# Kernel optimization log

Measured on AMD Instinct MI355X. Metric: run time of the kernel, lower is better.

## Reference

```python
import jax, jax.numpy as jnp
import numpy as np

B, S, D, H, HD, I = 8, 512, 2048, 32, 64, 8192
REL = 2 * 512 - 1  # 1023
EPS = 1e-6
SCALE = float(np.sqrt(HD))


def _layernorm(x, g, b):
    mu = jnp.mean(x, axis=-1, keepdims=True)
    var = jnp.mean(jnp.square(x - mu), axis=-1, keepdims=True)
    return (x - mu) / jnp.sqrt(var + EPS) * g + b


def setup_inputs() -> dict:
    key = jax.random.key(0)
    ks = jax.random.split(key, 10)
    s = 0.02
    return {
        "hidden_states": jax.random.normal(ks[0], (B, S, D), dtype=jnp.float32),
        "wq": jax.random.normal(ks[1], (D, D), dtype=jnp.float32) * s,
        "wk": jax.random.normal(ks[2], (D, D), dtype=jnp.float32) * s,
        "wv": jax.random.normal(ks[3], (D, D), dtype=jnp.float32) * s,
        "wo": jax.random.normal(ks[4], (D, D), dtype=jnp.float32) * s,
        "rel_pos": jax.random.normal(ks[5], (REL, HD), dtype=jnp.float32),
        "ln1_g": jnp.ones((D,), jnp.float32),
        "ln1_b": jnp.zeros((D,), jnp.float32),
        "gate_w": jax.random.normal(ks[6], (D, I), dtype=jnp.float32) * s,
        "up_w": jax.random.normal(ks[7], (D, I), dtype=jnp.float32) * s,
        "down_w": jax.random.normal(ks[8], (I, D), dtype=jnp.float32) * s,
        "ln2_g": jnp.ones((D,), jnp.float32),
        "ln2_b": jnp.zeros((D,), jnp.float32),
    }


def reference(hidden_states, wq, wk, wv, wo, rel_pos, ln1_g, ln1_b,
              gate_w, up_w, down_w, ln2_g, ln2_b):
    x = hidden_states
    # --- MultiHeadAttentionXL ---
    q = (x @ wq).reshape(B, S, H, HD)
    k = (x @ wk).reshape(B, S, H, HD)
    v = (x @ wv).reshape(B, S, H, HD)
    scores = jnp.einsum('bqhd,bkhd->bhqk', q, k) / SCALE
    # relative position bias (seq_len <= 512 path)
    pos = jnp.arange(S)
    rp = jnp.clip(pos[None, :] - pos[:, None] + 512 - 1, 0, REL - 1)  # [S,S]
    bias = rel_pos[rp].mean(axis=-1)  # [S,S]
    scores = scores + bias[None, None]
    attn = jax.nn.softmax(scores, axis=-1)
    ctx = jnp.einsum('bhqk,bkhd->bqhd', attn, v).reshape(B, S, D)
    attn_out = ctx @ wo
    # residual + post-LN
    h = _layernorm(x + attn_out, ln1_g, ln1_b)
    # --- FeedForwardXL (SwiGLU) ---
    gate = jax.nn.silu(h @ gate_w)
    up = h @ up_w
    ffn = (gate * up) @ down_w
    h = _layernorm(h + ffn, ln2_g, ln2_b)
    return h
```

## Files before the change

### kernel.cpp

```cpp
#include <hip/hip_runtime.h>
#include <cstdint>
#include <cstddef>

typedef _Float16 f16;
typedef _Float16 f16x8 __attribute__((ext_vector_type(8)));
typedef _Float16 f16x4 __attribute__((ext_vector_type(4)));
typedef float    f32x4 __attribute__((ext_vector_type(4)));

constexpr int S_ = 512, D_ = 2048, H_ = 32, HD_ = 64, I_ = 8192;
constexpr int M_ = 4096;
constexpr int IH_ = 4096;

enum { OP_F32 = 0, OP_QKT = 3, OP_PV = 4, OP_QKV = 6, OP_GU = 9, OP_ADD = 10 };

__device__ __forceinline__ void gl_lds16(const void* g, void* lds) {
  __builtin_amdgcn_global_load_lds(
      (const __attribute__((address_space(1))) void*)g,
      (__attribute__((address_space(3))) void*)lds, 16, 0, 0);
}

template <int BM, int BN, int WR, int WC, int OP>
__global__ __launch_bounds__(256, 2) void gemm_k(
    const f16* __restrict__ A, int lda,
    const f16* __restrict__ B, int ldb,
    void* __restrict__ Cp, int ldc,
    int K, int bh0, const float* __restrict__ relmean,
    const f16* __restrict__ B2) {
  constexpr int BK = 32;
  constexpr bool GU = (OP == OP_GU);
  constexpr int WM = BM / WR, WN = BN / WC;
  constexpr int IM = WM / 16, IN = WN / 16;
  constexpr int CA = BM / 64, CB = BN / 64;
  __shared__ __align__(16) f16 As[BM * BK];
  __shared__ __align__(16) f16 Bs[(GU ? 2 : 1) * BN * BK];
  const int tid = threadIdx.x, wave = tid >> 6, lane = tid & 63;
  const int wm = wave / WC, wn = wave % WC;
  const int bn = blockIdx.x, bm = blockIdx.y, bz = blockIdx.z;

  long aoff = 0, boff = 0;
  if constexpr (OP == OP_QKT) {
    int bh = bh0 + bz;
    long hb = (long)(bh >> 5) * (S_ * D_) + (long)(bh & (H_ - 1)) * HD_;
    aoff = hb; boff = hb;
  }
  if constexpr (OP == OP_PV) {
    int bh = bh0 + bz;
    aoff = (long)bz * S_ * S_;
    boff = (long)bh * HD_ * S_;
  }
  if constexpr (OP == OP_QKV) boff = (long)bz * D_ * D_;

  const f16* Ab = A + aoff + (long)bm * BM * lda;
  const f16* Bb = B + boff + (long)bn * BN * ldb;
  const f16* Bb2 = nullptr;
  if constexpr (GU) Bb2 = B2 + (long)bn * BN * ldb;

  f32x4 acc[IM][IN], acc2[IM][IN];
#pragma unroll
  for (int i = 0; i < IM; i++)
#pragma unroll
    for (int j = 0; j < IN; j++) {
      acc[i][j] = {0.f, 0.f, 0.f, 0.f};
      if constexpr (GU) acc2[i][j] = {0.f, 0.f, 0.f, 0.f};
    }

  const int lr = lane >> 2, l4 = lane & 3;
  const int q8 = (lane >> 4) * 8, l15 = lane & 15;

  for (int kt = 0; kt < K; kt += BK) {
#pragma unroll
    for (int c = 0; c < CA; c++) {
      int reg = wave * CA + c;
      gl_lds16(Ab + (long)(reg * 16 + lr) * lda + kt + l4 * 8, &As[reg * 512]);
    }
#pragma unroll
    for (int c = 0; c < CB; c++) {
      int reg = wave * CB + c;
      gl_lds16(Bb + (long)(reg * 16 + lr) * ldb + kt + l4 * 8, &Bs[reg * 512]);
      if constexpr (GU)
        gl_lds16(Bb2 + (long)(reg * 16 + lr) * ldb + kt + l4 * 8,
                 &Bs[BN * BK + reg * 512]);
    }
    __syncthreads();
    f16x8 af[IM], bf[IN], bf2[IN];
#pragma unroll
    for (int i = 0; i < IM; i++)
      af[i] = *(const f16x8*)&As[(wm * WM + i * 16 + l15) * BK + q8];
#pragma unroll
    for (int j = 0; j < IN; j++) {
      int colL = wn * WN + j * 16 + l15;
      bf[j] = *(const f16x8*)&Bs[colL * BK + q8];
      if constexpr (GU) bf2[j] = *(const f16x8*)&Bs[BN * BK + colL * BK + q8];
    }
#pragma unroll
    for (int i = 0; i < IM; i++)
#pragma unroll
      for (int j = 0; j < IN; j++) {
        acc[i][j] = __builtin_amdgcn_mfma_f32_16x16x32_f16(af[i], bf[j], acc[i][j], 0, 0, 0);
        if constexpr (GU)
          acc2[i][j] = __builtin_amdgcn_mfma_f32_16x16x32_f16(af[i], bf2[j], acc2[i][j], 0, 0, 0);
      }
    __syncthreads();
  }

  const int r0 = bm * BM + wm * WM + (lane >> 4) * 4;
  const int c0 = bn * BN + wn * WN + l15;
#pragma unroll
  for (int i = 0; i < IM; i++) {
#pragma unroll
    for (int j = 0; j < IN; j++) {
      int rowb = r0 + i * 16;
      int col = c0 + j * 16;
      if constexpr (OP == OP_F32) {
        float* C = (float*)Cp;
#pragma unroll
        for (int t = 0; t < 4; t++) C[(long)(rowb + t) * ldc + col] = acc[i][j][t];
      } else if constexpr (OP == OP_ADD) {
        float* C = (float*)Cp;
#pragma unroll
        for (int t = 0; t < 4; t++) C[(long)(rowb + t) * ldc + col] += acc[i][j][t];
      } else if constexpr (OP == OP_GU) {
        f16* C = (f16*)Cp;
#pragma unroll
        for (int t = 0; t < 4; t++) {
          float g = acc[i][j][t], u = acc2[i][j][t];
          C[(long)(rowb + t) * ldc + col] = (f16)(g / (1.f + __expf(-g)) * u);
        }
      } else if constexpr (OP == OP_QKT) {
        f16* C = (f16*)Cp + (long)bz * S_ * S_;
#pragma unroll
        for (int t = 0; t < 4; t++) {
          int r = rowb + t;
          C[(long)r * S_ + col] = (f16)(acc[i][j][t] * 0.125f + relmean[col - r + 511]);
        }
      } else if constexpr (OP == OP_PV) {
        int bh = bh0 + bz;
        f16* C = (f16*)Cp + (long)(bh >> 5) * (S_ * D_) + (long)(bh & (H_ - 1)) * HD_;
#pragma unroll
        for (int t = 0; t < 4; t++) C[(long)(rowb + t) * ldc + col] = (f16)acc[i][j][t];
      } else if constexpr (OP == OP_QKV) {
        f16* C = (f16*)Cp;
        if (bz < 2) {
          f16* Cq = C + (long)bz * M_ * D_;
#pragma unroll
          for (int t = 0; t < 4; t++) Cq[(long)(rowb + t) * ldc + col] = (f16)acc[i][j][t];
        } else {
          f16* Cv = C + (long)2 * M_ * D_;
          int b = rowb >> 9, s0 = rowb & 511, h = col >> 6, hd = col & 63;
          f16x4 pk;
#pragma unroll
          for (int t = 0; t < 4; t++) pk[t] = (f16)acc[i][j][t];
          *(f16x4*)&Cv[((long)(b * H_ + h) * HD_ + hd) * S_ + s0] = pk;
        }
      }
    }
  }
}

__global__ __launch_bounds__(256) void transpose_k(
    const float* __restrict__ in, int ldin, int k0, int n0,
    f16* __restrict__ out, int ldout) {
  __shared__ f16 t[64][68];
  const int kb = blockIdx.x * 64, nb = blockIdx.y * 64;
  const int tid = threadIdx.x;
  {
    const int kr = tid >> 4, nc = (tid & 15) * 4;
    const float* src = in + (long)(k0 + kb) * ldin + (n0 + nb);
#pragma unroll
    for (int i = 0; i < 4; i++) {
      int k = kr + i * 16;
      f32x4 v = *(const f32x4*)&src[(long)k * ldin + nc];
#pragma unroll
      for (int j = 0; j < 4; j++) t[nc + j][k] = (f16)v[j];
    }
  }
  __syncthreads();
  {
    const int n = tid >> 2, kc = (tid & 3) * 16;
    f16* dst = out + (long)(nb + n) * ldout + (kb + kc);
#pragma unroll
    for (int j = 0; j < 4; j++)
      *(f16x4*)&dst[j * 4] = *(const f16x4*)&t[n][kc + j * 4];
  }
}

__global__ void cvt_f16_k(const float* __restrict__ in, f16* __restrict__ out, int n4) {
  int i = blockIdx.x * 256 + threadIdx.x;
  if (i >= n4) return;
  f32x4 v = ((const f32x4*)in)[i];
  f16x4 o;
#pragma unroll
  for (int t = 0; t < 4; t++) o[t] = (f16)v[t];
  ((f16x4*)out)[i] = o;
}

__global__ void relmean_k(const float* __restrict__ rel, float* __restrict__ rm) {
  int i = blockIdx.x * 256 + threadIdx.x;
  if (i >= 1023) return;
  float s = 0.f;
#pragma unroll 8
  for (int d = 0; d < 64; d++) s += rel[i * 64 + d];
  rm[i] = s * (1.f / 64.f);
}

__global__ __launch_bounds__(256) void softmax_k(f16* __restrict__ Sc) {
  int r = blockIdx.x * 4 + (threadIdx.x >> 6);
  int lane = threadIdx.x & 63;
  f16* s = Sc + (long)r * S_;
  f16x8 d = *(const f16x8*)&s[lane * 8];
  float v[8], mx = -1e30f;
#pragma unroll
  for (int i = 0; i < 8; i++) { v[i] = (float)d[i]; mx = fmaxf(mx, v[i]); }
  for (int off = 32; off; off >>= 1) mx = fmaxf(mx, __shfl_xor(mx, off));
  float sum = 0.f;
#pragma unroll
  for (int i = 0; i < 8; i++) { v[i] = __expf(v[i] - mx); sum += v[i]; }
  for (int off = 32; off; off >>= 1) sum += __shfl_xor(sum, off);
  float rs = 1.f / sum;
  f16x8 o;
#pragma unroll
  for (int i = 0; i < 8; i++) o[i] = (f16)(v[i] * rs);
  *(f16x8*)&s[lane * 8] = o;
}

__global__ __launch_bounds__(256) void ln1_k(const float* __restrict__ X,
                                             const float* __restrict__ Y,
                                             const float* __restrict__ g,
                                             const float* __restrict__ b,
                                             f16* __restrict__ outH) {
  int row = blockIdx.x;
  const float* x = X + (long)row * D_;
  const float* y = Y + (long)row * D_;
  int t = threadIdx.x;
  float v[8], sum = 0.f, sq = 0.f;
#pragma unroll
  for (int i = 0; i < 8; i++) {
    int idx = t + i * 256;
    float val = x[idx] + y[idx];
    v[i] = val; sum += val; sq += val * val;
  }
  for (int off = 32; off; off >>= 1) { sum += __shfl_down(sum, off); sq += __shfl_down(sq, off); }
  __shared__ float s1[4], s2[4];
  if ((t & 63) == 0) { s1[t >> 6] = sum; s2[t >> 6] = sq; }
  __syncthreads();
  sum = s1[0] + s1[1] + s1[2] + s1[3];
  sq = s2[0] + s2[1] + s2[2] + s2[3];
  float mu = sum * (1.f / D_);
  float rstd = rsqrtf(sq * (1.f / D_) - mu * mu + 1e-6f);
#pragma unroll
  for (int i = 0; i < 8; i++) {
    int idx = t + i * 256;
    outH[(long)row * D_ + idx] = (f16)((v[i] - mu) * rstd * g[idx] + b[idx]);
  }
}

__global__ __launch_bounds__(256) void ln2f_k(const float* __restrict__ X,
                                              const f16* __restrict__ Y,
                                              const float* __restrict__ g,
                                              const float* __restrict__ b,
                                              float* __restrict__ outF) {
  int row = blockIdx.x;
  const float* x = X + (long)row * D_;
  const f16* y = Y + (long)row * D_;
  int t = threadIdx.x;
  float v[8], sum = 0.f, sq = 0.f;
#pragma unroll
  for (int i = 0; i < 8; i++) {
    int idx = t + i * 256;
    float val = x[idx] + (float)y[idx];
    v[i] = val; sum += val; sq += val * val;
  }
  for (int off = 32; off; off >>= 1) { sum += __shfl_down(sum, off); sq += __shfl_down(sq, off); }
  __shared__ float s1[4], s2[4];
  if ((t & 63) == 0) { s1[t >> 6] = sum; s2[t >> 6] = sq; }
  __syncthreads();
  sum = s1[0] + s1[1] + s1[2] + s1[3];
  sq = s2[0] + s2[1] + s2[2] + s2[3];
  float mu = sum * (1.f / D_);
  float rstd = rsqrtf(sq * (1.f / D_) - mu * mu + 1e-6f);
#pragma unroll
  for (int i = 0; i < 8; i++) {
    int idx = t + i * 256;
    outF[(long)row * D_ + idx] = (v[i] - mu) * rstd * g[idx] + b[idx];
  }
}

extern "C" void kernel_launch(void* const* d_in, const int* in_sizes, int n_in,
                              void* d_out, int out_size, void* d_ws, size_t ws_size,
                              hipStream_t stream) {
  const float* x    = (const float*)d_in[0];
  const float* wq   = (const float*)d_in[1];
  const float* wk   = (const float*)d_in[2];
  const float* wv   = (const float*)d_in[3];
  const float* wo   = (const float*)d_in[4];
  const float* rel  = (const float*)d_in[5];
  const float* ln1g = (const float*)d_in[6];
  const float* ln1b = (const float*)d_in[7];
  const float* gw   = (const float*)d_in[8];
  const float* uw   = (const float*)d_in[9];
  const float* dw   = (const float*)d_in[10];
  const float* ln2g = (const float*)d_in[11];
  const float* ln2b = (const float*)d_in[12];
  float* out = (float*)d_out;

  constexpr size_t MD2 = (size_t)M_ * D_ * 2;
  if (ws_size < 8 * MD2 + 4096) return;
  char* w = (char*)d_ws;
  f16* qb   = (f16*)(w + 0 * MD2);
  f16* vT   = (f16*)(w + 2 * MD2);
  f16* xb   = (f16*)(w + 3 * MD2);
  f16* sc   = (f16*)(w + 4 * MD2);
  f16* h1h  = (f16*)(w + 6 * MD2);
  f16* s7   = (f16*)(w + 7 * MD2);
  float* relmean = (float*)(w + 8 * MD2);
  f16* ctxb = xb;
  float* attn_out = (float*)qb;
  f16* wqT  = sc;
  f16* woT  = s7;
  f16* gwTh = qb;
  f16* uwTh = (f16*)(w + 1 * MD2);
  f16* gch  = vT;
  f16* dwTh = s7;
  float* facc = (float*)sc;

  cvt_f16_k<<<M_ * D_ / 4 / 256, 256, 0, stream>>>(x, xb, M_ * D_ / 4);
  relmean_k<<<4, 256, 0, stream>>>(rel, relmean);
  transpose_k<<<dim3(32, 32), 256, 0, stream>>>(wq, D_, 0, 0, wqT, D_);
  transpose_k<<<dim3(32, 32), 256, 0, stream>>>(wk, D_, 0, 0, wqT + (size_t)D_ * D_, D_);
  transpose_k<<<dim3(32, 32), 256, 0, stream>>>(wv, D_, 0, 0, wqT + 2 * (size_t)D_ * D_, D_);
  transpose_k<<<dim3(32, 32), 256, 0, stream>>>(wo, D_, 0, 0, woT, D_);

  gemm_k<128, 128, 2, 2, OP_QKV><<<dim3(16, 32, 3), 256, 0, stream>>>(
      xb, D_, wqT, D_, qb, D_, D_, 0, nullptr, nullptr);

  for (int c = 0; c < 4; c++) {
    int bh0 = c * 64;
    gemm_k<128, 128, 2, 2, OP_QKT><<<dim3(4, 4, 64), 256, 0, stream>>>(
        qb, D_, qb + (size_t)M_ * D_, D_, sc, S_, HD_, bh0, relmean, nullptr);
    softmax_k<<<64 * S_ / 4, 256, 0, stream>>>(sc);
    gemm_k<64, 64, 2, 2, OP_PV><<<dim3(1, 8, 64), 256, 0, stream>>>(
        sc, S_, vT, S_, ctxb, D_, S_, bh0, nullptr, nullptr);
  }

  gemm_k<128, 128, 2, 2, OP_F32><<<dim3(16, 32, 1), 256, 0, stream>>>(
      ctxb, D_, woT, D_, attn_out, D_, D_, 0, nullptr, nullptr);
  ln1_k<<<M_, 256, 0, stream>>>(x, attn_out, ln1g, ln1b, h1h);

  for (int h = 0; h < 2; h++) {
    transpose_k<<<dim3(32, 64), 256, 0, stream>>>(gw, I_, 0, h * IH_, gwTh, D_);
    transpose_k<<<dim3(32, 64), 256, 0, stream>>>(uw, I_, 0, h * IH_, uwTh, D_);
    transpose_k<<<dim3(64, 32), 256, 0, stream>>>(dw, D_, h * IH_, 0, dwTh, IH_);
    gemm_k<128, 64, 2, 2, OP_GU><<<dim3(IH_ / 64, 32, 1), 256, 0, stream>>>(
        h1h, D_, gwTh, D_, gch, IH_, D_, 0, nullptr, uwTh);
    if (h == 0)
      gemm_k<128, 128, 2, 2, OP_F32><<<dim3(16, 32, 1), 256, 0, stream>>>(
          gch, IH_, dwTh, IH_, facc, D_, IH_, 0, nullptr, nullptr);
    else
      gemm_k<128, 128, 2, 2, OP_ADD><<<dim3(16, 32, 1), 256, 0, stream>>>(
          gch, IH_, dwTh, IH_, facc, D_, IH_, 0, nullptr, nullptr);
  }
  ln2f_k<<<M_, 256, 0, stream>>>(facc, h1h, ln2g, ln2b, out);
}
```

Measured before the change: 1.249 ms.

## Add BK=64 swizzled LDS tiles for attention GEMMs and widen gate/up tile

Makes the GEMM K-tile depth a template parameter. A BK=64 variant uses an XOR-swizzled LDS layout to avoid bank conflicts, and the attention QK^T and PV GEMMs now use it. The end-of-loop barrier moves to the start of the next iteration. The gate/up SwiGLU GEMM goes from a 128x64 to a 128x128 tile with half the blocks, which raises reuse of the A tile. The larger tile doubles accumulators in the GU kernel, which risks register pressure and lower occupancy.

```diff
diff --git a/kernel.cpp b/kernel.cpp
--- a/kernel.cpp
+++ b/kernel.cpp
@@ -19,18 +19,22 @@
       (__attribute__((address_space(3))) void*)lds, 16, 0, 0);
 }
 
-template <int BM, int BN, int WR, int WC, int OP>
+template <int BM, int BN, int WR, int WC, int OP, int BK>
 __global__ __launch_bounds__(256, 2) void gemm_k(
     const f16* __restrict__ A, int lda,
     const f16* __restrict__ B, int ldb,
     void* __restrict__ Cp, int ldc,
     int K, int bh0, const float* __restrict__ relmean,
     const f16* __restrict__ B2) {
-  constexpr int BK = 32;
+  static_assert(WR * WC == 4, "4-wave blocks assumed");
+  static_assert(BK == 32 || BK == 64, "");
   constexpr bool GU = (OP == OP_GU);
   constexpr int WM = BM / WR, WN = BN / WC;
   constexpr int IM = WM / 16, IN = WN / 16;
-  constexpr int CA = BM / 64, CB = BN / 64;
+  constexpr int RR = (BK == 64) ? 8 : 16;
+  constexpr int CA = BM * BK / 2048;
+  constexpr int CB = BN * BK / 2048;
+  constexpr int KS = BK / 32;
   __shared__ __align__(16) f16 As[BM * BK];
   __shared__ __align__(16) f16 Bs[(GU ? 2 : 1) * BN * BK];
   const int tid = threadIdx.x, wave = tid >> 6, lane = tid & 63;
@@ -55,7 +59,7 @@
   const f16* Bb2 = nullptr;
   if constexpr (GU) Bb2 = B2 + (long)bn * BN * ldb;
 
-  f32x4 acc[IM][IN], acc2[IM][IN];
+  f32x4 acc[IM][IN], acc2[GU ? IM : 1][GU ? IN : 1];
 #pragma unroll
   for (int i = 0; i < IM; i++)
 #pragma unroll
@@ -64,43 +68,56 @@
       if constexpr (GU) acc2[i][j] = {0.f, 0.f, 0.f, 0.f};
     }
 
-  const int lr = lane >> 2, l4 = lane & 3;
-  const int q8 = (lane >> 4) * 8, l15 = lane & 15;
+  const int lrr = (BK == 64) ? (lane >> 3) : (lane >> 2);
+  const int lcc = (BK == 64) ? (lane & 7) : (lane & 3);
+  const int scc = (BK == 64) ? (lcc ^ (lrr & 7)) : lcc;
+  const int g = lane >> 4, l15 = lane & 15;
 
   for (int kt = 0; kt < K; kt += BK) {
+    if (kt) __syncthreads();
 #pragma unroll
     for (int c = 0; c < CA; c++) {
       int reg = wave * CA + c;
-      gl_lds16(Ab + (long)(reg * 16 + lr) * lda + kt + l4 * 8, &As[reg * 512]);
+      gl_lds16(Ab + (long)(reg * RR + lrr) * lda + kt + scc * 8, &As[reg * 512]);
     }
 #pragma unroll
     for (int c = 0; c < CB; c++) {
       int reg = wave * CB + c;
-      gl_lds16(Bb + (long)(reg * 16 + lr) * ldb + kt + l4 * 8, &Bs[reg * 512]);
+      gl_lds16(Bb + (long)(reg * RR + lrr) * ldb + kt + scc * 8, &Bs[reg * 512]);
       if constexpr (GU)
-        gl_lds16(Bb2 + (long)(reg * 16 + lr) * ldb + kt + l4 * 8,
+        gl_lds16(Bb2 + (long)(reg * RR + lrr) * ldb + kt + scc * 8,
                  &Bs[BN * BK + reg * 512]);
     }
     __syncthreads();
-    f16x8 af[IM], bf[IN], bf2[IN];
-#pragma unroll
-    for (int i = 0; i < IM; i++)
-      af[i] = *(const f16x8*)&As[(wm * WM + i * 16 + l15) * BK + q8];
-#pragma unroll
-    for (int j = 0; j < IN; j++) {
-      int colL = wn * WN + j * 16 + l15;
-      bf[j] = *(const f16x8*)&Bs[colL * BK + q8];
-      if constexpr (GU) bf2[j] = *(const f16x8*)&Bs[BN * BK + colL * BK + q8];
-    }
-#pragma unroll
-    for (int i = 0; i < IM; i++)
+    f16x8 af[KS][IM], bf[KS][IN], bf2[GU ? KS : 1][GU ? IN : 1];
+#pragma unroll
+    for (int s = 0; s < KS; s++) {
+#pragma unroll
+      for (int i = 0; i < IM; i++) {
+        int row = wm * WM + i * 16 + l15;
+        int cidx = s * 4 + g;
+        if constexpr (BK == 64) cidx ^= (row & 7);
+        af[s][i] = *(const f16x8*)&As[row * BK + cidx * 8];
+      }
 #pragma unroll
       for (int j = 0; j < IN; j++) {
-        acc[i][j] = __builtin_amdgcn_mfma_f32_16x16x32_f16(af[i], bf[j], acc[i][j], 0, 0, 0);
-        if constexpr (GU)
-          acc2[i][j] = __builtin_amdgcn_mfma_f32_16x16x32_f16(af[i], bf2[j], acc2[i][j], 0, 0, 0);
+        int colL = wn * WN + j * 16 + l15;
+        int cidx = s * 4 + g;
+        if constexpr (BK == 64) cidx ^= (colL & 7);
+        bf[s][j] = *(const f16x8*)&Bs[colL * BK + cidx * 8];
+        if constexpr (GU) bf2[s][j] = *(const f16x8*)&Bs[BN * BK + colL * BK + cidx * 8];
       }
-    __syncthreads();
+    }
+#pragma unroll
+    for (int s = 0; s < KS; s++)
+#pragma unroll
+      for (int i = 0; i < IM; i++)
+#pragma unroll
+        for (int j = 0; j < IN; j++) {
+          acc[i][j] = __builtin_amdgcn_mfma_f32_16x16x32_f16(af[s][i], bf[s][j], acc[i][j], 0, 0, 0);
+          if constexpr (GU)
+            acc2[i][j] = __builtin_amdgcn_mfma_f32_16x16x32_f16(af[s][i], bf2[s][j], acc2[i][j], 0, 0, 0);
+        }
   }
 
   const int r0 = bm * BM + wm * WM + (lane >> 4) * 4;
@@ -123,8 +140,8 @@
         f16* C = (f16*)Cp;
 #pragma unroll
         for (int t = 0; t < 4; t++) {
-          float g = acc[i][j][t], u = acc2[i][j][t];
-          C[(long)(rowb + t) * ldc + col] = (f16)(g / (1.f + __expf(-g)) * u);
+          float gg = acc[i][j][t], u = acc2[i][j][t];
+          C[(long)(rowb + t) * ldc + col] = (f16)(gg / (1.f + __expf(-gg)) * u);
         }
       } else if constexpr (OP == OP_QKT) {
         f16* C = (f16*)Cp + (long)bz * S_ * S_;
@@ -330,19 +347,19 @@
   transpose_k<<<dim3(32, 32), 256, 0, stream>>>(wv, D_, 0, 0, wqT + 2 * (size_t)D_ * D_, D_);
   transpose_k<<<dim3(32, 32), 256, 0, stream>>>(wo, D_, 0, 0, woT, D_);
 
-  gemm_k<128, 128, 2, 2, OP_QKV><<<dim3(16, 32, 3), 256, 0, stream>>>(
+  gemm_k<128, 128, 2, 2, OP_QKV, 32><<<dim3(16, 32, 3), 256, 0, stream>>>(
       xb, D_, wqT, D_, qb, D_, D_, 0, nullptr, nullptr);
 
   for (int c = 0; c < 4; c++) {
     int bh0 = c * 64;
-    gemm_k<128, 128, 2, 2, OP_QKT><<<dim3(4, 4, 64), 256, 0, stream>>>(
+    gemm_k<128, 128, 2, 2, OP_QKT, 64><<<dim3(4, 4, 64), 256, 0, stream>>>(
         qb, D_, qb + (size_t)M_ * D_, D_, sc, S_, HD_, bh0, relmean, nullptr);
     softmax_k<<<64 * S_ / 4, 256, 0, stream>>>(sc);
-    gemm_k<64, 64, 2, 2, OP_PV><<<dim3(1, 8, 64), 256, 0, stream>>>(
+    gemm_k<64, 64, 2, 2, OP_PV, 64><<<dim3(1, 8, 64), 256, 0, stream>>>(
         sc, S_, vT, S_, ctxb, D_, S_, bh0, nullptr, nullptr);
   }
 
-  gemm_k<128, 128, 2, 2, OP_F32><<<dim3(16, 32, 1), 256, 0, stream>>>(
+  gemm_k<128, 128, 2, 2, OP_F32, 32><<<dim3(16, 32, 1), 256, 0, stream>>>(
       ctxb, D_, woT, D_, attn_out, D_, D_, 0, nullptr, nullptr);
   ln1_k<<<M_, 256, 0, stream>>>(x, attn_out, ln1g, ln1b, h1h);
 
@@ -350,13 +367,13 @@
     transpose_k<<<dim3(32, 64), 256, 0, stream>>>(gw, I_, 0, h * IH_, gwTh, D_);
     transpose_k<<<dim3(32, 64), 256, 0, stream>>>(uw, I_, 0, h * IH_, uwTh, D_);
     transpose_k<<<dim3(64, 32), 256, 0, stream>>>(dw, D_, h * IH_, 0, dwTh, IH_);
-    gemm_k<128, 64, 2, 2, OP_GU><<<dim3(IH_ / 64, 32, 1), 256, 0, stream>>>(
+    gemm_k<128, 128, 2, 2, OP_GU, 32><<<dim3(IH_ / 128, 32, 1), 256, 0, stream>>>(
         h1h, D_, gwTh, D_, gch, IH_, D_, 0, nullptr, uwTh);
     if (h == 0)
-      gemm_k<128, 128, 2, 2, OP_F32><<<dim3(16, 32, 1), 256, 0, stream>>>(
+      gemm_k<128, 128, 2, 2, OP_F32, 32><<<dim3(16, 32, 1), 256, 0, stream>>>(
           gch, IH_, dwTh, IH_, facc, D_, IH_, 0, nullptr, nullptr);
     else
-      gemm_k<128, 128, 2, 2, OP_ADD><<<dim3(16, 32, 1), 256, 0, stream>>>(
+      gemm_k<128, 128, 2, 2, OP_ADD, 32><<<dim3(16, 32, 1), 256, 0, stream>>>(
           gch, IH_, dwTh, IH_, facc, D_, IH_, 0, nullptr, nullptr);
   }
   ln2f_k<<<M_, 256, 0, stream>>>(facc, h1h, ln2g, ln2b, out);
```

New measurement: 1.165 ms. -6.7%, faster.
